# Performance work log

Measured on AMD Instinct MI355X. Metric: run time of the kernel, lower is better.

## Reference

```python
import jax, jax.numpy as jnp
import numpy as np

B, T, IN, HID = 64, 512, 64, 256
NOISE_STD, TAU = 0.05, 0.2

def setup_inputs() -> dict:
    key = jax.random.key(0)
    ks = jax.random.split(key, 8)
    return {
        "u": jax.random.normal(ks[0], (B, T, IN), jnp.float32),
        "x0": jax.random.normal(ks[1], (B, HID), jnp.float32),
        "noise": jax.random.normal(ks[2], (T, B, HID), jnp.float32),
        "W_hh": jax.random.normal(ks[3], (HID, HID, HID), jnp.float32) * (0.1 / HID),
        "W_in": jax.random.normal(ks[4], (HID, IN), jnp.float32),
        "b_in": jnp.zeros((HID,), jnp.float32),
        "W_out": jax.random.normal(ks[5], (IN, HID), jnp.float32) * (1.0 / np.sqrt(HID)),
        "b_out": jnp.zeros((IN,), jnp.float32),
    }

def reference(u, x0, noise, W_hh, W_in, b_in, W_out, b_out):
    # form='rate', mode='cont': x <- x + std*n + tau*(-x + r W r + W_in u)
    def step(x, inp):
        u_t, n_t = inp                      # [B,IN], [B,HID]
        r = jnp.tanh(x)                     # rate form
        input_I = u_t @ W_in.T + b_in       # [B,HID]
        # bilinear form: hidden_W[b,i] = r[b,:] @ W_hh[i,:,:] @ r[b,:]
        hidden_W = jnp.einsum('bj,ijk,bk->bi', r, W_hh, r)
        x_new = x + NOISE_STD * n_t + TAU * (-x + hidden_W + input_I)
        return x_new, x_new
    u_t_first = jnp.transpose(u, (1, 0, 2))  # [T,B,IN]
    x_final, traj = jax.lax.scan(step, x0, (u_t_first, noise))
    trajectories = jnp.transpose(traj, (1, 0, 2))  # [B,T,HID]
    output = jnp.tanh(trajectories) @ W_out.T + b_out  # [B,T,IN]
    return output, x_final, trajectories
```

## Files before the change

### kernel.cpp

```cpp
#include <hip/hip_runtime.h>
#include <math.h>

#define B_   64
#define T_   512
#define IN_  64
#define HID_ 256
#define KTOT 65536

typedef __attribute__((ext_vector_type(8))) short  short8;
typedef __attribute__((ext_vector_type(4))) float  floatx4;

__device__ __forceinline__ unsigned short f2bf(float f) {
    unsigned int u = __float_as_uint(f);
    u += 0x7FFFu + ((u >> 16) & 1u);
    return (unsigned short)(u >> 16);
}
__device__ __forceinline__ float bf2f(unsigned short s) {
    return __uint_as_float(((unsigned int)s) << 16);
}

__device__ __forceinline__ void cstore(float* p, float v) {
    __hip_atomic_store(p, v, __ATOMIC_RELAXED, __HIP_MEMORY_SCOPE_AGENT);
}
__device__ __forceinline__ float cload(const float* p) {
    return __hip_atomic_load((float*)p, __ATOMIC_RELAXED, __HIP_MEMORY_SCOPE_AGENT);
}
__device__ __forceinline__ void cstore_u32(unsigned* p, unsigned v) {
    __hip_atomic_store(p, v, __ATOMIC_RELAXED, __HIP_MEMORY_SCOPE_AGENT);
}
__device__ __forceinline__ unsigned long long cload_u64(const unsigned long long* p) {
    return __hip_atomic_load((unsigned long long*)p, __ATOMIC_RELAXED,
                             __HIP_MEMORY_SCOPE_AGENT);
}

__device__ __forceinline__ size_t slot_off(int t) {
    return (size_t)(__brev((unsigned)t) >> 22) << 14;
}

__global__ __launch_bounds__(256) void conv_w(const float* __restrict__ W,
                                              unsigned short* __restrict__ Wb)
{
    const size_t idx = ((size_t)blockIdx.x * 256 + threadIdx.x) * 4;
    const float4 v = *(const float4*)(W + idx);
    unsigned int lo = (unsigned int)f2bf(v.x) | ((unsigned int)f2bf(v.y) << 16);
    unsigned int hi = (unsigned int)f2bf(v.z) | ((unsigned int)f2bf(v.w) << 16);
    *(uint2*)(Wb + idx) = make_uint2(lo, hi);
}

__global__ __launch_bounds__(256) void init_kernel(const float* __restrict__ x0,
                                                   const float* __restrict__ W_in,
                                                   unsigned short* __restrict__ rB,
                                                   float* __restrict__ W_inT,
                                                   unsigned* __restrict__ bar)
{
    const int b = blockIdx.x;
    const int i = threadIdx.x;
    rB[b * HID_ + i] = f2bf(tanhf(x0[b * HID_ + i]));
    W_inT[b * HID_ + i] = W_in[i * IN_ + b];
    if (b == 0) {
        for (int j2 = i; j2 < 2048; j2 += 256) bar[j2] = 0u;
    }
}

__global__ __launch_bounds__(256) void init_x(const float* __restrict__ x0,
                                              float* __restrict__ x)
{
    const int idx = blockIdx.x * 256 + threadIdx.x;
    x[idx] = x0[idx];
}

__global__ __launch_bounds__(256) void pre_kernel(const float* __restrict__ u,
                                                  const float* __restrict__ W_inT,
                                                  const float* __restrict__ b_in,
                                                  const float* __restrict__ noise,
                                                  float* __restrict__ pre)
{
    __shared__ float u_s[4][64];
    const int i  = threadIdx.x;
    const int b  = blockIdx.x >> 2;
    const int t0 = (blockIdx.x & 3) << 7;
    float wcol[64];
    #pragma unroll
    for (int k = 0; k < 64; ++k) wcol[k] = W_inT[(k << 8) + i];
    const float bi = b_in[i];
    for (int tt = 0; tt < 128; tt += 4) {
        __syncthreads();
        u_s[i >> 6][i & 63] = u[b * (T_ * IN_) + (t0 + tt + (i >> 6)) * IN_ + (i & 63)];
        __syncthreads();
        #pragma unroll
        for (int j2 = 0; j2 < 4; ++j2) {
            const int t = t0 + tt + j2;
            float acc = bi;
            #pragma unroll
            for (int k = 0; k < 64; ++k) acc = fmaf(u_s[j2][k], wcol[k], acc);
            pre[t * 16384 + b * HID_ + i] =
                fmaf(0.05f, noise[t * 16384 + b * HID_ + i], 0.2f * acc);
        }
    }
}

#define POISON_IDX 1600

__device__ __forceinline__ int spin_flag(unsigned* bar, int flag_idx, unsigned ep)
{
    int poison = 0;
    unsigned spins = 0;
    for (;;) {
        const unsigned f = __hip_atomic_load(&bar[flag_idx], __ATOMIC_RELAXED,
                                             __HIP_MEMORY_SCOPE_AGENT);
        if (f >= ep) break;
        if ((spins & 63u) == 0u) {
            if (__hip_atomic_load(&bar[POISON_IDX], __ATOMIC_RELAXED,
                                  __HIP_MEMORY_SCOPE_AGENT) != 0u) {
                poison = 1; break;
            }
        }
        if (++spins > 1000000u) {
            __hip_atomic_store(&bar[POISON_IDX], 1u, __ATOMIC_RELAXED,
                               __HIP_MEMORY_SCOPE_AGENT);
            poison = 1; break;
        }
        __builtin_amdgcn_s_sleep(1);
    }
    return poison;
}

__device__ __forceinline__ int grid_bar1(unsigned* bar, int pg, int cg,
                                         unsigned ep, int* abort_s)
{
    __syncthreads();
    if (threadIdx.x == 0) {
        const unsigned a = __hip_atomic_fetch_add(&bar[pg * 32], 1u,
                               __ATOMIC_RELAXED, __HIP_MEMORY_SCOPE_AGENT);
        if (a == ep * 64u - 1u) {
            __hip_atomic_store(&bar[256 + pg * 32], ep, __ATOMIC_RELAXED,
                               __HIP_MEMORY_SCOPE_AGENT);
        }
        *abort_s = spin_flag(bar, 256 + cg * 32, ep);
    }
    __syncthreads();
    return *abort_s;
}

__device__ __forceinline__ int grid_bar2(unsigned* bar, int g2,
                                         unsigned ep, int* abort_s)
{
    __syncthreads();
    if (threadIdx.x == 0) {
        const unsigned a = __hip_atomic_fetch_add(&bar[512 + g2 * 32], 1u,
                               __ATOMIC_RELAXED, __HIP_MEMORY_SCOPE_AGENT);
        if (a == ep * 32u - 1u) {
            const unsigned r = __hip_atomic_fetch_add(&bar[1024], 1u,
                                   __ATOMIC_RELAXED, __HIP_MEMORY_SCOPE_AGENT);
            if (r == ep * 16u - 1u) {
                #pragma unroll
                for (int g = 0; g < 16; ++g)
                    __hip_atomic_store(&bar[1056 + g * 32], ep, __ATOMIC_RELAXED,
                                       __HIP_MEMORY_SCOPE_AGENT);
            }
        }
        *abort_s = spin_flag(bar, 1056 + g2 * 32, ep);
    }
    __syncthreads();
    return *abort_s;
}

__global__ __launch_bounds__(256, 2) void persist4(
    const float* __restrict__ W_hh,
    unsigned short* __restrict__ ring,
    float* __restrict__ P,
    const float* __restrict__ pre,
    const float* __restrict__ u,
    const float* __restrict__ W_inT,
    const float* __restrict__ b_in,
    const float* __restrict__ noise,
    const float* __restrict__ x0,
    float* __restrict__ traj,
    float* __restrict__ xf,
    unsigned* bar,
    int use_pre)
{
    __shared__ unsigned short rL[16384];
    __shared__ float Wr[3][4][64][4];
    __shared__ float red[128];
    __shared__ int abort_s;

    const int tid = threadIdx.x;
    const int l   = tid & 63;
    const int w   = tid >> 6;
    const int m   = l & 15;
    const int q   = l >> 4;
    const int blk = blockIdx.x;
    const int ig  = blk >> 5;
    const int kg  = blk & 31;
    const int i0  = ig << 4;
    const int j0  = (kg << 3) + (w << 1);

    const int pg = blk >> 6;
    const int cg = blk & 7;
    const int g2 = blk >> 5;

    short8 wv[16];
    {
        const float* s0 = W_hh + (size_t)(i0 + m) * KTOT + (j0 << 8) + (q << 3);
        #pragma unroll
        for (int kc = 0; kc < 8; ++kc) {
            #pragma unroll
            for (int half = 0; half < 2; ++half) {
                const float* sp = s0 + (half << 8) + (kc << 5);
                const float4 a  = *(const float4*)(sp);
                const float4 bv = *(const float4*)(sp + 4);
                unsigned* gp = (unsigned*)&wv[kc + (half << 3)];
                gp[0] = (unsigned)f2bf(a.x)  | ((unsigned)f2bf(a.y)  << 16);
                gp[1] = (unsigned)f2bf(a.z)  | ((unsigned)f2bf(a.w)  << 16);
                gp[2] = (unsigned)f2bf(bv.x) | ((unsigned)f2bf(bv.y) << 16);
                gp[3] = (unsigned)f2bf(bv.z) | ((unsigned)f2bf(bv.w) << 16);
            }
        }
    }

    const int own   = tid & 31;
    const int pair0 = blk << 5;
    const int sgrp  = tid >> 5;
    const int cb    = (pair0 + own) >> 8;
    const int ci    = (pair0 + own) & 255;
    float x_reg = x0[pair0 + own];

    const floatx4 z4 = {0.f, 0.f, 0.f, 0.f};

    float pn_pref = 0.f;
    if (use_pre) pn_pref = pre[pair0 + own];

    for (int t = 0; t < T_; ++t) {
        {
            const uint4* src = (const uint4*)(ring + slot_off(t));
            #pragma unroll
            for (int j2 = 0; j2 < 8; ++j2) {
                const int u4  = (j2 << 8) + tid;
                const uint4 v = src[u4];
                const int row = u4 >> 5;
                const int c8  = (u4 & 31) << 3;
                *(uint4*)&rL[(row << 8) + (c8 ^ ((row & 7) << 3))] = v;
            }
        }
        __syncthreads();

        floatx4 aA[4], aB[4];
        #pragma unroll
        for (int mt = 0; mt < 4; ++mt) { aA[mt] = z4; aB[mt] = z4; }

        #pragma unroll
        for (int kc = 0; kc < 8; ++kc) {
            const int cc = (q << 3) + (kc << 5);
            #pragma unroll
            for (int mt = 0; mt < 4; ++mt) {
                const int row = (mt << 4) + m;
                const short8 af = *(const short8*)&rL[(row << 8) + (cc ^ ((row & 7) << 3))];
                aA[mt] = __builtin_amdgcn_mfma_f32_16x16x32_bf16(af, wv[kc],     aA[mt], 0, 0, 0);
                aB[mt] = __builtin_amdgcn_mfma_f32_16x16x32_bf16(af, wv[kc + 8], aB[mt], 0, 0, 0);
            }
        }

        floatx4 pd[4];
        #pragma unroll
        for (int mt = 0; mt < 4; ++mt) {
            #pragma unroll
            for (int reg = 0; reg < 4; ++reg) {
                const int b = (mt << 4) + (q << 2) + reg;
                const unsigned rr = *(const unsigned*)&rL[(b << 8) + (j0 ^ ((b & 7) << 3))];
                pd[mt][reg] = bf2f((unsigned short)(rr & 0xffffu)) * aA[mt][reg]
                            + bf2f((unsigned short)(rr >> 16))     * aB[mt][reg];
            }
        }

        if (w > 0) {
            #pragma unroll
            for (int mt = 0; mt < 4; ++mt) *(floatx4*)&Wr[w - 1][mt][l][0] = pd[mt];
        }
        __syncthreads();
        if (w == 0) {
            #pragma unroll
            for (int mt = 0; mt < 4; ++mt) {
                floatx4 s = pd[mt];
                s += *(const floatx4*)&Wr[0][mt][l][0];
                s += *(const floatx4*)&Wr[1][mt][l][0];
                s += *(const floatx4*)&Wr[2][mt][l][0];
                #pragma unroll
                for (int reg = 0; reg < 4; ++reg) {
                    const int b = (mt << 4) + (q << 2) + reg;
                    cstore(&P[(kg << 14) + (b << 8) + i0 + m], s[reg]);
                }
            }
        }

        if (grid_bar1(bar, pg, cg, (unsigned)(t + 1), &abort_s)) break;

        {
            const float* Pp = P + (size_t)(sgrp << 2) * 16384 + pair0 + own;
            float part = cload(Pp) + cload(Pp + 16384)
                       + cload(Pp + 2 * 16384) + cload(Pp + 3 * 16384);
            part += __shfl_xor(part, 32, 64);
            if ((tid & 32) == 0) red[(w << 5) + own] = part;
            __syncthreads();
            const float hidden = red[own] + red[32 + own] + red[64 + own] + red[96 + own];

            float pn;
            if (use_pre) {
                pn = pn_pref;
            } else {
                float inp = b_in[ci];
                const float* ur = u + cb * (T_ * IN_) + (t << 6);
                #pragma unroll
                for (int k = 0; k < 64; ++k)
                    inp = fmaf(ur[k], W_inT[(k << 8) + ci], inp);
                pn = fmaf(0.05f, noise[((size_t)t << 14) + pair0 + own], 0.2f * inp);
            }
            const float xn = fmaf(0.8f, x_reg, fmaf(0.2f, hidden, pn));
            x_reg = xn;

            const unsigned short rb = f2bf(tanhf(xn));
            const unsigned nb = (unsigned)__shfl_xor((int)(unsigned)rb, 1, 64);
            if (tid < 32) {
                traj[(size_t)cb * (T_ * HID_) + (t << 8) + ci] = xn;
                if ((own & 1) == 0) {
                    cstore_u32((unsigned*)(ring + slot_off(t + 1))
                                   + ((pair0 + own) >> 1),
                               ((unsigned)rb) | (nb << 16));
                }
                if (t == T_ - 1) xf[pair0 + own] = xn;
            }
            if (use_pre && t + 1 < T_) pn_pref = pre[((t + 1) << 14) + pair0 + own];
        }

        if (grid_bar2(bar, g2, (unsigned)(t + 1), &abort_s)) break;
    }
}

__device__ __forceinline__ int grid_bar_old(unsigned* bar, int gid, unsigned ep,
                                            int* abort_s)
{
    __syncthreads();
    if (threadIdx.x == 0) {
        const unsigned a = __hip_atomic_fetch_add(&bar[512 + gid * 32], 1u,
                               __ATOMIC_RELAXED, __HIP_MEMORY_SCOPE_AGENT);
        if (a == ep * 32u - 1u) {
            const unsigned r = __hip_atomic_fetch_add(&bar[1024], 1u,
                                   __ATOMIC_RELAXED, __HIP_MEMORY_SCOPE_AGENT);
            if (r == ep * 16u - 1u) {
                #pragma unroll
                for (int g = 0; g < 16; ++g)
                    __hip_atomic_store(&bar[1056 + g * 32], ep, __ATOMIC_RELAXED,
                                       __HIP_MEMORY_SCOPE_AGENT);
            }
        }
        *abort_s = spin_flag(bar, 1056 + gid * 32, ep);
    }
    __syncthreads();
    return *abort_s;
}

__global__ __launch_bounds__(256, 2) void persist_kernel(
    const float* __restrict__ W_hh,
    unsigned short* __restrict__ ring,
    float* __restrict__ P,
    const float* __restrict__ pre,
    const float* __restrict__ u,
    const float* __restrict__ W_inT,
    const float* __restrict__ b_in,
    const float* __restrict__ noise,
    const float* __restrict__ x0,
    float* __restrict__ traj,
    float* __restrict__ xf,
    unsigned* bar,
    int use_pre)
{
    __shared__ unsigned short rL[16384];
    __shared__ float Wr[3][4][64][4];
    __shared__ float red[128];
    __shared__ int abort_s;

    const int tid = threadIdx.x;
    const int l   = tid & 63;
    const int w   = tid >> 6;
    const int m   = l & 15;
    const int q   = l >> 4;
    const int blk = blockIdx.x;
    const int ig  = blk >> 5;
    const int kg  = blk & 31;
    const int i0  = ig << 4;
    const int j0  = (kg << 3) + (w << 1);

    short8 wv[16];
    {
        const float* s0 = W_hh + (size_t)(i0 + m) * KTOT + (j0 << 8) + (q << 3);
        #pragma unroll
        for (int kc = 0; kc < 8; ++kc) {
            #pragma unroll
            for (int half = 0; half < 2; ++half) {
                const float* sp = s0 + (half << 8) + (kc << 5);
                const float4 a = *(const float4*)(sp);
                const float4 bv = *(const float4*)(sp + 4);
                unsigned* gp = (unsigned*)&wv[kc + (half << 3)];
                gp[0] = (unsigned)f2bf(a.x)  | ((unsigned)f2bf(a.y)  << 16);
                gp[1] = (unsigned)f2bf(a.z)  | ((unsigned)f2bf(a.w)  << 16);
                gp[2] = (unsigned)f2bf(bv.x) | ((unsigned)f2bf(bv.y) << 16);
                gp[3] = (unsigned)f2bf(bv.z) | ((unsigned)f2bf(bv.w) << 16);
            }
        }
    }

    const int own   = tid & 31;
    const int pair0 = blk << 5;
    const int sgrp  = tid >> 5;
    const int cb    = (pair0 + own) >> 8;
    const int ci    = (pair0 + own) & 255;
    float x_reg = x0[pair0 + own];

    const int gid = blk >> 5;
    const floatx4 z4 = {0.f, 0.f, 0.f, 0.f};

    for (int t = 0; t < T_; ++t) {
        {
            unsigned long long* src = (unsigned long long*)(ring + (size_t)t * 16384);
            #pragma unroll
            for (int j2 = 0; j2 < 16; ++j2) {
                const int u2 = (j2 << 8) + tid;
                const unsigned long long v = cload_u64(&src[u2]);
                const int row = u2 >> 6;
                const int c4  = (u2 & 63) << 2;
                *(unsigned long long*)&rL[(row << 8) + (c4 ^ ((row & 7) << 3))] = v;
            }
        }
        __syncthreads();

        floatx4 aA[4], aB[4];
        #pragma unroll
        for (int mt = 0; mt < 4; ++mt) { aA[mt] = z4; aB[mt] = z4; }

        #pragma unroll
        for (int kc = 0; kc < 8; ++kc) {
            const int cc = (q << 3) + (kc << 5);
            #pragma unroll
            for (int mt = 0; mt < 4; ++mt) {
                const int row = (mt << 4) + m;
                const short8 af = *(const short8*)&rL[(row << 8) + (cc ^ ((row & 7) << 3))];
                aA[mt] = __builtin_amdgcn_mfma_f32_16x16x32_bf16(af, wv[kc],     aA[mt], 0, 0, 0);
                aB[mt] = __builtin_amdgcn_mfma_f32_16x16x32_bf16(af, wv[kc + 8], aB[mt], 0, 0, 0);
            }
        }

        floatx4 pd[4];
        #pragma unroll
        for (int mt = 0; mt < 4; ++mt) {
            #pragma unroll
            for (int reg = 0; reg < 4; ++reg) {
                const int b = (mt << 4) + (q << 2) + reg;
                const unsigned rr = *(const unsigned*)&rL[(b << 8) + (j0 ^ ((b & 7) << 3))];
                pd[mt][reg] = bf2f((unsigned short)(rr & 0xffffu)) * aA[mt][reg]
                            + bf2f((unsigned short)(rr >> 16))     * aB[mt][reg];
            }
        }

        if (w > 0) {
            #pragma unroll
            for (int mt = 0; mt < 4; ++mt) *(floatx4*)&Wr[w - 1][mt][l][0] = pd[mt];
        }
        __syncthreads();
        if (w == 0) {
            #pragma unroll
            for (int mt = 0; mt < 4; ++mt) {
                floatx4 s = pd[mt];
                s += *(const floatx4*)&Wr[0][mt][l][0];
                s += *(const floatx4*)&Wr[1][mt][l][0];
                s += *(const floatx4*)&Wr[2][mt][l][0];
                #pragma unroll
                for (int reg = 0; reg < 4; ++reg) {
                    const int b = (mt << 4) + (q << 2) + reg;
                    cstore(&P[(kg << 14) + (b << 8) + i0 + m], s[reg]);
                }
            }
        }

        if (grid_bar_old(bar, gid, (unsigned)(2 * t + 1), &abort_s)) break;

        {
            const float* Pp = P + (size_t)(sgrp << 2) * 16384 + pair0 + own;
            float part = cload(Pp) + cload(Pp + 16384)
                       + cload(Pp + 2 * 16384) + cload(Pp + 3 * 16384);
            part += __shfl_xor(part, 32, 64);
            if ((tid & 32) == 0) red[(w << 5) + own] = part;
            __syncthreads();
            const float hidden = red[own] + red[32 + own] + red[64 + own] + red[96 + own];

            float pn;
            if (use_pre) {
                pn = pre[(t << 14) + pair0 + own];
            } else {
                float inp = b_in[ci];
                const float* ur = u + cb * (T_ * IN_) + (t << 6);
                #pragma unroll
                for (int k = 0; k < 64; ++k)
                    inp = fmaf(ur[k], W_inT[(k << 8) + ci], inp);
                pn = fmaf(0.05f, noise[((size_t)t << 14) + pair0 + own], 0.2f * inp);
            }
            const float xn = fmaf(0.8f, x_reg, fmaf(0.2f, hidden, pn));
            x_reg = xn;

            const unsigned short rb = f2bf(tanhf(xn));
            const unsigned nb = (unsigned)__shfl_xor((int)(unsigned)rb, 1, 64);
            if (tid < 32) {
                traj[(size_t)cb * (T_ * HID_) + (t << 8) + ci] = xn;
                if ((own & 1) == 0) {
                    cstore_u32((unsigned*)(ring + (size_t)(t + 1) * 16384)
                                   + ((pair0 + own) >> 1),
                               ((unsigned)rb) | (nb << 16));
                }
                if (t == T_ - 1) xf[pair0 + own] = xn;
            }
        }

        if (grid_bar_old(bar, gid, (unsigned)(2 * t + 2), &abort_s)) break;
    }
}

__global__ __launch_bounds__(256) void gemm_step(const unsigned short* __restrict__ Wb,
                                                 const unsigned short* __restrict__ rB,
                                                 float* __restrict__ P)
{
    __shared__ unsigned short A_lds[32768];

    const int tid = threadIdx.x;
    const int l   = tid & 63;
    const int w   = tid >> 6;
    const int m   = l & 15;
    const int q   = l >> 4;
    const int ig  = blockIdx.x >> 7;
    const int c   = blockIdx.x & 127;
    const int i0  = ig << 6;

    {
        const unsigned short* src = Wb + (size_t)(i0 + (w << 4) + m) * KTOT
                                       + (c << 9) + (q << 3);
        unsigned short* dst = &A_lds[(w << 13) + (l << 3)];
        #pragma unroll
        for (int kc = 0; kc < 16; ++kc) {
            uint4 v = *(const uint4*)(src + (kc << 5));
            *(uint4*)(dst + (kc << 9)) = v;
        }
    }

    const int b = (w << 4) + m;
    const float rj0 = bf2f(rB[b * HID_ + 2 * c]);
    const float rj1 = bf2f(rB[b * HID_ + 2 * c + 1]);
    const unsigned short* rrow = rB + b * HID_ + (q << 3);

    floatx4 acc0 = {0.f, 0.f, 0.f, 0.f};
    floatx4 acc1 = {0.f, 0.f, 0.f, 0.f};
    floatx4 acc2 = {0.f, 0.f, 0.f, 0.f};
    floatx4 acc3 = {0.f, 0.f, 0.f, 0.f};

    __syncthreads();

    #pragma unroll
    for (int kc = 0; kc < 16; ++kc) {
        const float rj = (kc < 8) ? rj0 : rj1;
        const uint4 rv = *(const uint4*)(rrow + ((kc & 7) << 5));
        short8 gfrag;
        {
            unsigned int* gp = (unsigned int*)&gfrag;
            const unsigned short* rs = (const unsigned short*)&rv;
            #pragma unroll
            for (int p = 0; p < 4; ++p) {
                const float lo = bf2f(rs[2 * p])     * rj;
                const float hi = bf2f(rs[2 * p + 1]) * rj;
                gp[p] = (unsigned int)f2bf(lo) | ((unsigned int)f2bf(hi) << 16);
            }
        }
        const unsigned short* ab = &A_lds[(kc << 9) + (l << 3)];
        const short8 w0 = *(const short8*)(ab);
        const short8 w1 = *(const short8*)(ab + 8192);
        const short8 w2 = *(const short8*)(ab + 16384);
        const short8 w3 = *(const short8*)(ab + 24576);
        acc0 = __builtin_amdgcn_mfma_f32_16x16x32_bf16(gfrag, w0, acc0, 0, 0, 0);
        acc1 = __builtin_amdgcn_mfma_f32_16x16x32_bf16(gfrag, w1, acc1, 0, 0, 0);
        acc2 = __builtin_amdgcn_mfma_f32_16x16x32_bf16(gfrag, w2, acc2, 0, 0, 0);
        acc3 = __builtin_amdgcn_mfma_f32_16x16x32_bf16(gfrag, w3, acc3, 0, 0, 0);
    }

    #pragma unroll
    for (int reg = 0; reg < 4; ++reg) {
        float* dst = P + (c << 14) + ((w << 4) + (q << 2) + reg) * HID_ + i0 + m;
        dst[0]  = acc0[reg];
        dst[16] = acc1[reg];
        dst[32] = acc2[reg];
        dst[48] = acc3[reg];
    }
}

__global__ __launch_bounds__(64) void combine_step(const float* __restrict__ P,
                                                   const float* __restrict__ noise,
                                                   const float* __restrict__ u,
                                                   const float* __restrict__ W_inT,
                                                   const float* __restrict__ b_in,
                                                   float* __restrict__ x,
                                                   unsigned short* __restrict__ rB,
                                                   float* __restrict__ traj,
                                                   int t)
{
    const int b = blockIdx.x >> 2;
    const int i = ((blockIdx.x & 3) << 6) + threadIdx.x;

    __shared__ float u_s[64];
    u_s[threadIdx.x] = u[b * (T_ * IN_) + t * IN_ + threadIdx.x];
    __syncthreads();

    const float* Pp = P + b * HID_ + i;
    float s0 = 0.f, s1 = 0.f, s2 = 0.f, s3 = 0.f;
    #pragma unroll 4
    for (int cc = 0; cc < 128; cc += 4) {
        s0 += Pp[(cc + 0) * 16384];
        s1 += Pp[(cc + 1) * 16384];
        s2 += Pp[(cc + 2) * 16384];
        s3 += Pp[(cc + 3) * 16384];
    }
    const float hidden = (s0 + s1) + (s2 + s3);

    float inp = b_in[i];
    #pragma unroll
    for (int k = 0; k < 64; ++k) inp += u_s[k] * W_inT[k * HID_ + i];

    const float xo = x[b * HID_ + i];
    const float n  = noise[t * (B_ * HID_) + b * HID_ + i];
    const float xn = 0.8f * xo + 0.05f * n + 0.2f * (hidden + inp);

    x[b * HID_ + i] = xn;
    traj[(size_t)b * (T_ * HID_) + t * HID_ + i] = xn;
    rB[b * HID_ + i] = f2bf(tanhf(xn));
}

__global__ __launch_bounds__(256) void copy_xfinal(const float* __restrict__ x,
                                                   float* __restrict__ xf)
{
    const int idx = blockIdx.x * 256 + threadIdx.x;
    xf[idx] = x[idx];
}

__global__ __launch_bounds__(256) void output_kernel(const float* __restrict__ traj,
                                                     const float* __restrict__ W_out,
                                                     const float* __restrict__ b_out,
                                                     float* __restrict__ out)
{
    __shared__ float r_s[16 * 256];
    __shared__ float Wt[64 * 65];

    const int tid = threadIdx.x;
    const int b   = blockIdx.x >> 5;
    const int t0  = (blockIdx.x & 31) << 4;

    #pragma unroll
    for (int r = 0; r < 16; ++r) {
        r_s[r * 256 + tid] = tanhf(traj[(size_t)b * (T_ * HID_) + (t0 + r) * HID_ + tid]);
    }

    const int o  = tid & 63;
    const int rg = tid >> 6;
    float acc0 = b_out[o];
    float acc1 = acc0, acc2 = acc0, acc3 = acc0;

    for (int ib = 0; ib < 4; ++ib) {
        __syncthreads();
        #pragma unroll
        for (int r = 0; r < 16; ++r) {
            const int f  = (r << 8) + tid;
            const int oo = f >> 6;
            const int il = f & 63;
            Wt[il * 65 + oo] = W_out[oo * 256 + (ib << 6) + il];
        }
        __syncthreads();
        #pragma unroll 16
        for (int il = 0; il < 64; ++il) {
            const float ww = Wt[il * 65 + o];
            const int i = (ib << 6) + il;
            acc0 += r_s[(rg * 4 + 0) * 256 + i] * ww;
            acc1 += r_s[(rg * 4 + 1) * 256 + i] * ww;
            acc2 += r_s[(rg * 4 + 2) * 256 + i] * ww;
            acc3 += r_s[(rg * 4 + 3) * 256 + i] * ww;
        }
    }
    float* ob = out + b * (T_ * IN_) + (t0 + (rg << 2)) * IN_ + o;
    ob[0 * IN_] = acc0;
    ob[1 * IN_] = acc1;
    ob[2 * IN_] = acc2;
    ob[3 * IN_] = acc3;
}

extern "C" void kernel_launch(void* const* d_in, const int* in_sizes, int n_in,
                              void* d_out, int out_size, void* d_ws, size_t ws_size,
                              hipStream_t stream)
{
    const float* u     = (const float*)d_in[0];
    const float* x0    = (const float*)d_in[1];
    const float* noise = (const float*)d_in[2];
    const float* W_hh  = (const float*)d_in[3];
    const float* W_in  = (const float*)d_in[4];
    const float* b_in  = (const float*)d_in[5];
    const float* W_out = (const float*)d_in[6];
    const float* b_out = (const float*)d_in[7];

    float* out  = (float*)d_out;
    float* xf   = out + 2097152;
    float* traj = out + 2097152 + 16384;

    char* wsb = (char*)d_ws;
    float*          P     = (float*)(wsb);
    unsigned short* ring  = (unsigned short*)(wsb + 8388608ull);
    unsigned short* Wb    = (unsigned short*)(wsb + 8388608ull);
    float*          W_inT = (float*)(wsb + 41943040ull);
    unsigned*       bar   = (unsigned*)(wsb + 42008576ull);
    unsigned short* rB_fb = (unsigned short*)(wsb + 42016768ull);
    float*          x     = (float*)(wsb + 42049536ull);
    float*          pre   = (float*)(wsb + 42115072ull);
    const int use_pre = (ws_size >= 42115072ull + 33554432ull) ? 1 : 0;

    init_kernel<<<64, 256, 0, stream>>>(x0, W_in, ring, W_inT, bar);
    if (use_pre) pre_kernel<<<256, 256, 0, stream>>>(u, W_inT, b_in, noise, pre);

    {
        const float*          a_W    = W_hh;
        unsigned short*       a_ring = ring;
        float*                a_P    = P;
        const float*          a_pre  = pre;
        const float*          a_u    = u;
        const float*          a_WinT = W_inT;
        const float*          a_bin  = b_in;
        const float*          a_nz   = noise;
        const float*          a_x0   = x0;
        float*                a_traj = traj;
        float*                a_xf   = xf;
        unsigned*             a_bar  = bar;
        int                   a_up   = use_pre;
        void* args[] = { &a_W, &a_ring, &a_P, &a_pre, &a_u, &a_WinT, &a_bin,
                         &a_nz, &a_x0, &a_traj, &a_xf, &a_bar, &a_up };
        hipError_t e = hipLaunchCooperativeKernel(persist4, dim3(512), dim3(256),
                                                  args, 0, stream);
        if (e == hipSuccess) {
            output_kernel<<<2048, 256, 0, stream>>>(traj, W_out, b_out, out);
            return;
        }
    }

    {
        const float*          a_W    = W_hh;
        unsigned short*       a_ring = ring;
        float*                a_P    = P;
        const float*          a_pre  = pre;
        const float*          a_u    = u;
        const float*          a_WinT = W_inT;
        const float*          a_bin  = b_in;
        const float*          a_nz   = noise;
        const float*          a_x0   = x0;
        float*                a_traj = traj;
        float*                a_xf   = xf;
        unsigned*             a_bar  = bar;
        int                   a_up   = use_pre;
        void* args[] = { &a_W, &a_ring, &a_P, &a_pre, &a_u, &a_WinT, &a_bin,
                         &a_nz, &a_x0, &a_traj, &a_xf, &a_bar, &a_up };
        hipError_t e = hipLaunchCooperativeKernel(persist_kernel, dim3(512), dim3(256),
                                                  args, 0, stream);
        if (e == hipSuccess) {
            output_kernel<<<2048, 256, 0, stream>>>(traj, W_out, b_out, out);
            return;
        }
    }

    {
        conv_w<<<16384, 256, 0, stream>>>(W_hh, Wb);
        init_kernel<<<64, 256, 0, stream>>>(x0, W_in, rB_fb, W_inT, bar);
        init_x<<<64, 256, 0, stream>>>(x0, x);
        for (int t = 0; t < T_; ++t) {
            gemm_step<<<512, 256, 0, stream>>>(Wb, rB_fb, P);
            combine_step<<<256, 64, 0, stream>>>(P, noise, u, W_inT, b_in, x, rB_fb, traj, t);
        }
        copy_xfinal<<<64, 256, 0, stream>>>(x, xf);
        output_kernel<<<2048, 256, 0, stream>>>(traj, W_out, b_out, out);
    }
}
```

Baseline: 4.740 ms.

## Add 512-thread persistent kernel with group-local partial barrier and 8-wave reduction

Adds persist5, a cooperative persistent kernel using 256 blocks of 512 threads, so each block covers 16 j-columns across 8 waves. The first barrier of each step now synchronises only the 16 blocks sharing an output row group, and a separate hierarchical barrier closes the step. Partial sums are reduced over 7 wave slices in LDS, and then over 16 k-groups read from global memory. The aim is fewer blocks contending on barriers and fewer partial-sum slices per step. In exchange it needs more LDS per block, allows only one block per CU, and reorders the barrier counters. The launch order now tries persist5 before persist4, and the older persist_kernel is removed.

```diff
diff --git a/kernel.cpp b/kernel.cpp
--- a/kernel.cpp
+++ b/kernel.cpp
@@ -27,10 +27,6 @@
 }
 __device__ __forceinline__ void cstore_u32(unsigned* p, unsigned v) {
     __hip_atomic_store(p, v, __ATOMIC_RELAXED, __HIP_MEMORY_SCOPE_AGENT);
-}
-__device__ __forceinline__ unsigned long long cload_u64(const unsigned long long* p) {
-    return __hip_atomic_load((unsigned long long*)p, __ATOMIC_RELAXED,
-                             __HIP_MEMORY_SCOPE_AGENT);
 }
 
 __device__ __forceinline__ size_t slot_off(int t) {
@@ -99,7 +95,7 @@
     }
 }
 
-#define POISON_IDX 1600
+#define POISON_IDX 1824
 
 __device__ __forceinline__ int spin_flag(unsigned* bar, int flag_idx, unsigned ep)
 {
@@ -123,6 +119,212 @@
         __builtin_amdgcn_s_sleep(1);
     }
     return poison;
+}
+
+__device__ __forceinline__ int bar1_ig(unsigned* bar, int g, unsigned ep,
+                                       int* abort_s)
+{
+    __syncthreads();
+    if (threadIdx.x == 0) {
+        const unsigned a = __hip_atomic_fetch_add(&bar[g * 32], 1u,
+                               __ATOMIC_RELAXED, __HIP_MEMORY_SCOPE_AGENT);
+        if (a == ep * 16u - 1u)
+            __hip_atomic_store(&bar[512 + g * 32], ep, __ATOMIC_RELAXED,
+                               __HIP_MEMORY_SCOPE_AGENT);
+        *abort_s = spin_flag(bar, 512 + g * 32, ep);
+    }
+    __syncthreads();
+    return *abort_s;
+}
+
+__device__ __forceinline__ int bar2_all(unsigned* bar, int g, unsigned ep,
+                                        int* abort_s)
+{
+    __syncthreads();
+    if (threadIdx.x == 0) {
+        const unsigned a = __hip_atomic_fetch_add(&bar[1024 + g * 32], 1u,
+                               __ATOMIC_RELAXED, __HIP_MEMORY_SCOPE_AGENT);
+        if (a == ep * 16u - 1u) {
+            const unsigned r = __hip_atomic_fetch_add(&bar[1536], 1u,
+                                   __ATOMIC_RELAXED, __HIP_MEMORY_SCOPE_AGENT);
+            if (r == ep * 16u - 1u) {
+                #pragma unroll
+                for (int gg = 0; gg < 16; ++gg)
+                    __hip_atomic_store(&bar[1568 + gg * 16], ep, __ATOMIC_RELAXED,
+                                       __HIP_MEMORY_SCOPE_AGENT);
+            }
+        }
+        *abort_s = spin_flag(bar, 1568 + g * 16, ep);
+    }
+    __syncthreads();
+    return *abort_s;
+}
+
+__global__ __launch_bounds__(512, 1) void persist5(
+    const float* __restrict__ W_hh,
+    unsigned short* __restrict__ ring,
+    float* __restrict__ P,
+    const float* __restrict__ pre,
+    const float* __restrict__ u,
+    const float* __restrict__ W_inT,
+    const float* __restrict__ b_in,
+    const float* __restrict__ noise,
+    const float* __restrict__ x0,
+    float* __restrict__ traj,
+    float* __restrict__ xf,
+    unsigned* bar,
+    int use_pre)
+{
+    __shared__ unsigned short rL[16384];
+    __shared__ float Wr[7][4][64][4];
+    __shared__ float red[8][64];
+    __shared__ int abort_s;
+
+    const int tid = threadIdx.x;
+    const int l   = tid & 63;
+    const int w   = tid >> 6;
+    const int m   = l & 15;
+    const int q   = l >> 4;
+    const int blk = blockIdx.x;
+    const int ig  = blk >> 4;
+    const int kg4 = blk & 15;
+    const int i0  = ig << 4;
+    const int j0  = (kg4 << 4) + (w << 1);
+
+    short8 wv[16];
+    {
+        const float* s0 = W_hh + (size_t)(i0 + m) * KTOT + (j0 << 8) + (q << 3);
+        #pragma unroll
+        for (int kc = 0; kc < 8; ++kc) {
+            #pragma unroll
+            for (int half = 0; half < 2; ++half) {
+                const float* sp = s0 + (half << 8) + (kc << 5);
+                const float4 a  = *(const float4*)(sp);
+                const float4 bv = *(const float4*)(sp + 4);
+                unsigned* gp = (unsigned*)&wv[kc + (half << 3)];
+                gp[0] = (unsigned)f2bf(a.x)  | ((unsigned)f2bf(a.y)  << 16);
+                gp[1] = (unsigned)f2bf(a.z)  | ((unsigned)f2bf(a.w)  << 16);
+                gp[2] = (unsigned)f2bf(bv.x) | ((unsigned)f2bf(bv.y) << 16);
+                gp[3] = (unsigned)f2bf(bv.z) | ((unsigned)f2bf(bv.w) << 16);
+            }
+        }
+    }
+
+    const int p       = l;
+    const int cb      = (kg4 << 2) + (p >> 4);
+    const int ci      = i0 + (p & 15);
+    const int pairIdx = (cb << 8) + ci;
+    float x_reg = (w == 0) ? x0[pairIdx] : 0.f;
+
+    float pn_pref = 0.f;
+    if (use_pre && w == 0) pn_pref = pre[pairIdx];
+
+    const int g = ig;
+    const floatx4 z4 = {0.f, 0.f, 0.f, 0.f};
+
+    for (int t = 0; t < T_; ++t) {
+        {
+            const uint4* src = (const uint4*)(ring + slot_off(t));
+            #pragma unroll
+            for (int j2 = 0; j2 < 4; ++j2) {
+                const int u4  = (j2 << 9) + tid;
+                const uint4 v = src[u4];
+                const int row = u4 >> 5;
+                const int c8  = (u4 & 31) << 3;
+                *(uint4*)&rL[(row << 8) + (c8 ^ ((row & 7) << 3))] = v;
+            }
+        }
+        __syncthreads();
+
+        floatx4 aA[4], aB[4];
+        #pragma unroll
+        for (int mt = 0; mt < 4; ++mt) { aA[mt] = z4; aB[mt] = z4; }
+
+        #pragma unroll
+        for (int kc = 0; kc < 8; ++kc) {
+            const int cc = (q << 3) + (kc << 5);
+            #pragma unroll
+            for (int mt = 0; mt < 4; ++mt) {
+                const int row = (mt << 4) + m;
+                const short8 af = *(const short8*)&rL[(row << 8) + (cc ^ ((row & 7) << 3))];
+                aA[mt] = __builtin_amdgcn_mfma_f32_16x16x32_bf16(af, wv[kc],     aA[mt], 0, 0, 0);
+                aB[mt] = __builtin_amdgcn_mfma_f32_16x16x32_bf16(af, wv[kc + 8], aB[mt], 0, 0, 0);
+            }
+        }
+
+        floatx4 pd[4];
+        #pragma unroll
+        for (int mt = 0; mt < 4; ++mt) {
+            #pragma unroll
+            for (int reg = 0; reg < 4; ++reg) {
+                const int b = (mt << 4) + (q << 2) + reg;
+                const unsigned rr = *(const unsigned*)&rL[(b << 8) + (j0 ^ ((b & 7) << 3))];
+                pd[mt][reg] = bf2f((unsigned short)(rr & 0xffffu)) * aA[mt][reg]
+                            + bf2f((unsigned short)(rr >> 16))     * aB[mt][reg];
+            }
+        }
+
+        if (w > 0) {
+            #pragma unroll
+            for (int mt = 0; mt < 4; ++mt) *(floatx4*)&Wr[w - 1][mt][l][0] = pd[mt];
+        }
+        __syncthreads();
+        if (w == 0) {
+            #pragma unroll
+            for (int mt = 0; mt < 4; ++mt) {
+                floatx4 s = pd[mt];
+                #pragma unroll
+                for (int k = 0; k < 7; ++k)
+                    s += *(const floatx4*)&Wr[k][mt][l][0];
+                #pragma unroll
+                for (int reg = 0; reg < 4; ++reg) {
+                    const int b = (mt << 4) + (q << 2) + reg;
+                    cstore(&P[(kg4 << 14) + (b << 8) + i0 + m], s[reg]);
+                }
+            }
+        }
+
+        if (bar1_ig(bar, g, (unsigned)(t + 1), &abort_s)) break;
+
+        {
+            const int sp = tid >> 6;
+            const int pr = tid & 63;
+            const int b2 = (kg4 << 2) + (pr >> 4);
+            const int i2 = i0 + (pr & 15);
+            const float* Pp = P + (size_t)(sp << 1) * 16384 + (b2 << 8) + i2;
+            red[sp][pr] = cload(Pp) + cload(Pp + 16384);
+        }
+        __syncthreads();
+        if (w == 0) {
+            const float hidden = ((red[0][p] + red[1][p]) + (red[2][p] + red[3][p]))
+                               + ((red[4][p] + red[5][p]) + (red[6][p] + red[7][p]));
+            float pn;
+            if (use_pre) {
+                pn = pn_pref;
+            } else {
+                float inp = b_in[ci];
+                const float* ur = u + cb * (T_ * IN_) + (t << 6);
+                #pragma unroll
+                for (int k = 0; k < 64; ++k)
+                    inp = fmaf(ur[k], W_inT[(k << 8) + ci], inp);
+                pn = fmaf(0.05f, noise[((size_t)t << 14) + pairIdx], 0.2f * inp);
+            }
+            const float xn = fmaf(0.8f, x_reg, fmaf(0.2f, hidden, pn));
+            x_reg = xn;
+
+            const unsigned short rb = f2bf(tanhf(xn));
+            const unsigned nb = (unsigned)__shfl_xor((int)(unsigned)rb, 1, 64);
+            if ((p & 1) == 0) {
+                cstore_u32((unsigned*)(ring + slot_off(t + 1)) + (pairIdx >> 1),
+                           ((unsigned)rb) | (nb << 16));
+            }
+            traj[(size_t)cb * (T_ * HID_) + (t << 8) + ci] = xn;
+            if (t == T_ - 1) xf[pairIdx] = xn;
+            if (use_pre && t + 1 < T_) pn_pref = pre[((t + 1) << 14) + pairIdx];
+        }
+
+        if (bar2_all(bar, g, (unsigned)(t + 1), &abort_s)) break;
+    }
 }
 
 __device__ __forceinline__ int grid_bar1(unsigned* bar, int pg, int cg,
@@ -336,193 +538,6 @@
     }
 }
 
-__device__ __forceinline__ int grid_bar_old(unsigned* bar, int gid, unsigned ep,
-                                            int* abort_s)
-{
-    __syncthreads();
-    if (threadIdx.x == 0) {
-        const unsigned a = __hip_atomic_fetch_add(&bar[512 + gid * 32], 1u,
-                               __ATOMIC_RELAXED, __HIP_MEMORY_SCOPE_AGENT);
-        if (a == ep * 32u - 1u) {
-            const unsigned r = __hip_atomic_fetch_add(&bar[1024], 1u,
-                                   __ATOMIC_RELAXED, __HIP_MEMORY_SCOPE_AGENT);
-            if (r == ep * 16u - 1u) {
-                #pragma unroll
-                for (int g = 0; g < 16; ++g)
-                    __hip_atomic_store(&bar[1056 + g * 32], ep, __ATOMIC_RELAXED,
-                                       __HIP_MEMORY_SCOPE_AGENT);
-            }
-        }
-        *abort_s = spin_flag(bar, 1056 + gid * 32, ep);
-    }
-    __syncthreads();
-    return *abort_s;
-}
-
-__global__ __launch_bounds__(256, 2) void persist_kernel(
-    const float* __restrict__ W_hh,
-    unsigned short* __restrict__ ring,
-    float* __restrict__ P,
-    const float* __restrict__ pre,
-    const float* __restrict__ u,
-    const float* __restrict__ W_inT,
-    const float* __restrict__ b_in,
-    const float* __restrict__ noise,
-    const float* __restrict__ x0,
-    float* __restrict__ traj,
-    float* __restrict__ xf,
-    unsigned* bar,
-    int use_pre)
-{
-    __shared__ unsigned short rL[16384];
-    __shared__ float Wr[3][4][64][4];
-    __shared__ float red[128];
-    __shared__ int abort_s;
-
-    const int tid = threadIdx.x;
-    const int l   = tid & 63;
-    const int w   = tid >> 6;
-    const int m   = l & 15;
-    const int q   = l >> 4;
-    const int blk = blockIdx.x;
-    const int ig  = blk >> 5;
-    const int kg  = blk & 31;
-    const int i0  = ig << 4;
-    const int j0  = (kg << 3) + (w << 1);
-
-    short8 wv[16];
-    {
-        const float* s0 = W_hh + (size_t)(i0 + m) * KTOT + (j0 << 8) + (q << 3);
-        #pragma unroll
-        for (int kc = 0; kc < 8; ++kc) {
-            #pragma unroll
-            for (int half = 0; half < 2; ++half) {
-                const float* sp = s0 + (half << 8) + (kc << 5);
-                const float4 a = *(const float4*)(sp);
-                const float4 bv = *(const float4*)(sp + 4);
-                unsigned* gp = (unsigned*)&wv[kc + (half << 3)];
-                gp[0] = (unsigned)f2bf(a.x)  | ((unsigned)f2bf(a.y)  << 16);
-                gp[1] = (unsigned)f2bf(a.z)  | ((unsigned)f2bf(a.w)  << 16);
-                gp[2] = (unsigned)f2bf(bv.x) | ((unsigned)f2bf(bv.y) << 16);
-                gp[3] = (unsigned)f2bf(bv.z) | ((unsigned)f2bf(bv.w) << 16);
-            }
-        }
-    }
-
-    const int own   = tid & 31;
-    const int pair0 = blk << 5;
-    const int sgrp  = tid >> 5;
-    const int cb    = (pair0 + own) >> 8;
-    const int ci    = (pair0 + own) & 255;
-    float x_reg = x0[pair0 + own];
-
-    const int gid = blk >> 5;
-    const floatx4 z4 = {0.f, 0.f, 0.f, 0.f};
-
-    for (int t = 0; t < T_; ++t) {
-        {
-            unsigned long long* src = (unsigned long long*)(ring + (size_t)t * 16384);
-            #pragma unroll
-            for (int j2 = 0; j2 < 16; ++j2) {
-                const int u2 = (j2 << 8) + tid;
-                const unsigned long long v = cload_u64(&src[u2]);
-                const int row = u2 >> 6;
-                const int c4  = (u2 & 63) << 2;
-                *(unsigned long long*)&rL[(row << 8) + (c4 ^ ((row & 7) << 3))] = v;
-            }
-        }
-        __syncthreads();
-
-        floatx4 aA[4], aB[4];
-        #pragma unroll
-        for (int mt = 0; mt < 4; ++mt) { aA[mt] = z4; aB[mt] = z4; }
-
-        #pragma unroll
-        for (int kc = 0; kc < 8; ++kc) {
-            const int cc = (q << 3) + (kc << 5);
-            #pragma unroll
-            for (int mt = 0; mt < 4; ++mt) {
-                const int row = (mt << 4) + m;
-                const short8 af = *(const short8*)&rL[(row << 8) + (cc ^ ((row & 7) << 3))];
-                aA[mt] = __builtin_amdgcn_mfma_f32_16x16x32_bf16(af, wv[kc],     aA[mt], 0, 0, 0);
-                aB[mt] = __builtin_amdgcn_mfma_f32_16x16x32_bf16(af, wv[kc + 8], aB[mt], 0, 0, 0);
-            }
-        }
-
-        floatx4 pd[4];
-        #pragma unroll
-        for (int mt = 0; mt < 4; ++mt) {
-            #pragma unroll
-            for (int reg = 0; reg < 4; ++reg) {
-                const int b = (mt << 4) + (q << 2) + reg;
-                const unsigned rr = *(const unsigned*)&rL[(b << 8) + (j0 ^ ((b & 7) << 3))];
-                pd[mt][reg] = bf2f((unsigned short)(rr & 0xffffu)) * aA[mt][reg]
-                            + bf2f((unsigned short)(rr >> 16))     * aB[mt][reg];
-            }
-        }
-
-        if (w > 0) {
-            #pragma unroll
-            for (int mt = 0; mt < 4; ++mt) *(floatx4*)&Wr[w - 1][mt][l][0] = pd[mt];
-        }
-        __syncthreads();
-        if (w == 0) {
-            #pragma unroll
-            for (int mt = 0; mt < 4; ++mt) {
-                floatx4 s = pd[mt];
-                s += *(const floatx4*)&Wr[0][mt][l][0];
-                s += *(const floatx4*)&Wr[1][mt][l][0];
-                s += *(const floatx4*)&Wr[2][mt][l][0];
-                #pragma unroll
-                for (int reg = 0; reg < 4; ++reg) {
-                    const int b = (mt << 4) + (q << 2) + reg;
-                    cstore(&P[(kg << 14) + (b << 8) + i0 + m], s[reg]);
-                }
-            }
-        }
-
-        if (grid_bar_old(bar, gid, (unsigned)(2 * t + 1), &abort_s)) break;
-
-        {
-            const float* Pp = P + (size_t)(sgrp << 2) * 16384 + pair0 + own;
-            float part = cload(Pp) + cload(Pp + 16384)
-                       + cload(Pp + 2 * 16384) + cload(Pp + 3 * 16384);
-            part += __shfl_xor(part, 32, 64);
-            if ((tid & 32) == 0) red[(w << 5) + own] = part;
-            __syncthreads();
-            const float hidden = red[own] + red[32 + own] + red[64 + own] + red[96 + own];
-
-            float pn;
-            if (use_pre) {
-                pn = pre[(t << 14) + pair0 + own];
-            } else {
-                float inp = b_in[ci];
-                const float* ur = u + cb * (T_ * IN_) + (t << 6);
-                #pragma unroll
-                for (int k = 0; k < 64; ++k)
-                    inp = fmaf(ur[k], W_inT[(k << 8) + ci], inp);
-                pn = fmaf(0.05f, noise[((size_t)t << 14) + pair0 + own], 0.2f * inp);
-            }
-            const float xn = fmaf(0.8f, x_reg, fmaf(0.2f, hidden, pn));
-            x_reg = xn;
-
-            const unsigned short rb = f2bf(tanhf(xn));
-            const unsigned nb = (unsigned)__shfl_xor((int)(unsigned)rb, 1, 64);
-            if (tid < 32) {
-                traj[(size_t)cb * (T_ * HID_) + (t << 8) + ci] = xn;
-                if ((own & 1) == 0) {
-                    cstore_u32((unsigned*)(ring + (size_t)(t + 1) * 16384)
-                                   + ((pair0 + own) >> 1),
-                               ((unsigned)rb) | (nb << 16));
-                }
-                if (t == T_ - 1) xf[pair0 + own] = xn;
-            }
-        }
-
-        if (grid_bar_old(bar, gid, (unsigned)(2 * t + 2), &abort_s)) break;
-    }
-}
-
 __global__ __launch_bounds__(256) void gemm_step(const unsigned short* __restrict__ Wb,
                                                  const unsigned short* __restrict__ rB,
                                                  float* __restrict__ P)
@@ -570,10 +585,10 @@
             unsigned int* gp = (unsigned int*)&gfrag;
             const unsigned short* rs = (const unsigned short*)&rv;
             #pragma unroll
-            for (int p = 0; p < 4; ++p) {
-                const float lo = bf2f(rs[2 * p])     * rj;
-                const float hi = bf2f(rs[2 * p + 1]) * rj;
-                gp[p] = (unsigned int)f2bf(lo) | ((unsigned int)f2bf(hi) << 16);
+            for (int pp = 0; pp < 4; ++pp) {
+                const float lo = bf2f(rs[2 * pp])     * rj;
+                const float hi = bf2f(rs[2 * pp + 1]) * rj;
+                gp[pp] = (unsigned int)f2bf(lo) | ((unsigned int)f2bf(hi) << 16);
             }
         }
         const unsigned short* ab = &A_lds[(kc << 9) + (l << 3)];
@@ -724,6 +739,30 @@
 
     init_kernel<<<64, 256, 0, stream>>>(x0, W_in, ring, W_inT, bar);
     if (use_pre) pre_kernel<<<256, 256, 0, stream>>>(u, W_inT, b_in, noise, pre);
+
+    {
+        const float*          a_W    = W_hh;
+        unsigned short*       a_ring = ring;
+        float*                a_P    = P;
+        const float*          a_pre  = pre;
+        const float*          a_u    = u;
+        const float*          a_WinT = W_inT;
+        const float*          a_bin  = b_in;
+        const float*          a_nz   = noise;
+        const float*          a_x0   = x0;
+        float*                a_traj = traj;
+        float*                a_xf   = xf;
+        unsigned*             a_bar  = bar;
+        int                   a_up   = use_pre;
+        void* args[] = { &a_W, &a_ring, &a_P, &a_pre, &a_u, &a_WinT, &a_bin,
+                         &a_nz, &a_x0, &a_traj, &a_xf, &a_bar, &a_up };
+        hipError_t e = hipLaunchCooperativeKernel(persist5, dim3(256), dim3(512),
+                                                  args, 0, stream);
+        if (e == hipSuccess) {
+            output_kernel<<<2048, 256, 0, stream>>>(traj, W_out, b_out, out);
+            return;
+        }
+    }
 
     {
         const float*          a_W    = W_hh;
@@ -750,30 +789,6 @@
     }
 
     {
-        const float*          a_W    = W_hh;
-        unsigned short*       a_ring = ring;
-        float*                a_P    = P;
-        const float*          a_pre  = pre;
-        const float*          a_u    = u;
-        const float*          a_WinT = W_inT;
-        const float*          a_bin  = b_in;
-        const float*          a_nz   = noise;
-        const float*          a_x0   = x0;
-        float*                a_traj = traj;
-        float*                a_xf   = xf;
-        unsigned*             a_bar  = bar;
-        int                   a_up   = use_pre;
-        void* args[] = { &a_W, &a_ring, &a_P, &a_pre, &a_u, &a_WinT, &a_bin,
-                         &a_nz, &a_x0, &a_traj, &a_xf, &a_bar, &a_up };
-        hipError_t e = hipLaunchCooperativeKernel(persist_kernel, dim3(512), dim3(256),
-                                                  args, 0, stream);
-        if (e == hipSuccess) {
-            output_kernel<<<2048, 256, 0, stream>>>(traj, W_out, b_out, out);
-            return;
-        }
-    }
-
-    {
         conv_w<<<16384, 256, 0, stream>>>(W_hh, Wb);
         init_kernel<<<64, 256, 0, stream>>>(x0, W_in, rB_fb, W_inT, bar);
         init_x<<<64, 256, 0, stream>>>(x0, x);
```

After: 3.977 ms. 1.19x faster.
